# Kernel tuning notes

Hardware: AMD Instinct MI355X
Metric: run time of the kernel (lower is better)

Reference implementation:

```python
import jax, jax.numpy as jnp
import numpy as np

N_NODES = 100000
N_EDGES = 3200000
N_GRAPHS = 64
DIMS = [512, 1024, 512, 256, 128, 64, 32]
N_CLASSES = 10


def setup_inputs() -> dict:
    key = jax.random.key(0)
    ks = jax.random.split(key, 20)
    inp = {}
    inp['h'] = jax.random.normal(ks[0], (N_NODES, DIMS[0]), dtype=jnp.float32)
    inp['src'] = jax.random.randint(ks[1], (N_EDGES,), 0, N_NODES, dtype=jnp.int32)
    inp['dst'] = jax.random.randint(ks[2], (N_EDGES,), 0, N_NODES, dtype=jnp.int32)
    inp['graph_ids'] = jnp.sort(jax.random.randint(ks[3], (N_NODES,), 0, N_GRAPHS, dtype=jnp.int32))
    # GraphConv weights (glorot-like) and biases for the 6 layers
    for i in range(6):
        fi, fo = DIMS[i], DIMS[i + 1]
        scale = jnp.sqrt(2.0 / (fi + fo)).astype(jnp.float32)
        inp[f'W{i+1}'] = jax.random.normal(ks[4 + i], (fi, fo), dtype=jnp.float32) * scale
        inp[f'b{i+1}'] = jnp.zeros((fo,), dtype=jnp.float32)
    inp['Wc'] = jax.random.normal(ks[12], (DIMS[-1], N_CLASSES), dtype=jnp.float32) * 0.1
    inp['bc'] = jnp.zeros((N_CLASSES,), dtype=jnp.float32)
    return inp


def _graph_conv(h, W, b, src, dst, out_inv_sqrt, in_inv_sqrt):
    """DGL GraphConv, norm='both': D_dst^{-1/2} A (D_src^{-1/2} h) W + b.
    Apply W first when it shrinks the feature dim (DGL's mult-first trick)."""
    fi, fo = W.shape
    if fi > fo:
        h = h @ W  # shrink before aggregating
    h = h * out_inv_sqrt[:, None]
    agg = jax.ops.segment_sum(h[src], dst, num_segments=N_NODES)  # SpMM
    agg = agg * in_inv_sqrt[:, None]
    if fi <= fo:
        agg = agg @ W
    return agg + b


def reference(h, src, dst, graph_ids, W1, b1, W2, b2, W3, b3, W4, b4, W5, b5, W6, b6, Wc, bc):
    ones_e = jnp.ones((N_EDGES,), dtype=jnp.float32)
    out_deg = jax.ops.segment_sum(ones_e, src, num_segments=N_NODES)
    in_deg = jax.ops.segment_sum(ones_e, dst, num_segments=N_NODES)
    out_inv_sqrt = jax.lax.rsqrt(jnp.clip(out_deg, 1.0))  # allow_zero_in_degree -> clamp
    in_inv_sqrt = jax.lax.rsqrt(jnp.clip(in_deg, 1.0))
    for (W, b) in [(W1, b1), (W2, b2), (W3, b3), (W4, b4), (W5, b5), (W6, b6)]:
        h = jax.nn.relu(_graph_conv(h, W, b, src, dst, out_inv_sqrt, in_inv_sqrt))
    # dgl.mean_nodes over batched graph
    sums = jax.ops.segment_sum(h, graph_ids, num_segments=N_GRAPHS)
    counts = jax.ops.segment_sum(jnp.ones((N_NODES,), jnp.float32), graph_ids, num_segments=N_GRAPHS)
    hg = sums / jnp.clip(counts, 1.0)[:, None]
    return hg @ Wc + bc  # [N_GRAPHS, n_classes]
```

## Files before the change

### kernel.cpp

```cpp
#include <hip/hip_runtime.h>

#define N_NODES 100000
#define N_EDGES 3200000
#define N_GRAPHS 64
#define M_PAD   100096
#define CAP     128

typedef unsigned short u16;
typedef __bf16 bf16x8 __attribute__((ext_vector_type(8)));
typedef float f32x4 __attribute__((ext_vector_type(4)));
typedef unsigned int u32x4 __attribute__((ext_vector_type(4)));
typedef __attribute__((address_space(3))) unsigned int lds_u32;
typedef __attribute__((address_space(1))) unsigned int glb_u32;

__device__ inline u16 f2bf(float f) {
  unsigned u = __float_as_uint(f);
  unsigned r = (u + 0x7fffu + ((u >> 16) & 1u)) >> 16;
  return (u16)r;
}
__device__ inline float bf2f(u16 h) {
  return __uint_as_float(((unsigned)h) << 16);
}

__global__ void k_build(const int* __restrict__ src, const int* __restrict__ dst,
                        int* __restrict__ odeg, int* __restrict__ cur,
                        int* __restrict__ colp) {
  int e = blockIdx.x * blockDim.x + threadIdx.x;
  if (e < N_EDGES) {
    int s = src[e], d = dst[e];
    atomicAdd(&odeg[s], 1);
    int pos = atomicAdd(&cur[d], 1);
    if (pos < CAP) colp[(size_t)d * CAP + pos] = s;
  }
}

__global__ void k_rsqrt(const int* __restrict__ odeg, const int* __restrict__ ideg,
                        float* __restrict__ a, float* __restrict__ bI) {
  int v = blockIdx.x * blockDim.x + threadIdx.x;
  if (v < N_NODES) {
    a[v]  = rsqrtf(fmaxf((float)odeg[v], 1.0f));
    bI[v] = rsqrtf(fmaxf((float)ideg[v], 1.0f));
  }
}

__global__ void k_prep(const float* __restrict__ x, const float* __restrict__ ascl,
                       u16* __restrict__ y) {
  int i = blockIdx.x * blockDim.x + threadIdx.x;
  if (i >= N_NODES * 128) return;
  int row = i >> 7;
  float s = ascl[row];
  float4 v = ((const float4*)x)[i];
  uint2 o;
  o.x = (unsigned)f2bf(v.x * s) | ((unsigned)f2bf(v.y * s) << 16);
  o.y = (unsigned)f2bf(v.z * s) | ((unsigned)f2bf(v.w * s) << 16);
  ((uint2*)y)[i] = o;
}

__global__ void k_wt(const float* __restrict__ W, u16* __restrict__ Wt, int fi, int fo) {
  int idx = blockIdx.x * blockDim.x + threadIdx.x;
  if (idx >= fi * fo) return;
  int n = idx / fi, k = idx % fi;
  Wt[idx] = f2bf(W[(size_t)k * fo + n]);
}

template<int BM, int BN, int WM, int WN>
__global__ __launch_bounds__(256) void k_mfma(
    const u16* __restrict__ A, const u16* __restrict__ Wt,
    const float* __restrict__ bias, const float* __restrict__ rowscale,
    u16* __restrict__ C, int N, int K, int flags)
{
  constexpr int BK = 32;
  constexpr int WX = BN / WN;
  constexpr int WY = BM / WM;
  static_assert(WX * WY == 4, "4 waves");
  constexpr int TM = WM / 16;
  constexpr int TN = WN / 16;
  constexpr int CA = BM / 16;
  constexpr int CB = BN / 16;

  __shared__ __align__(1024) u16 As[BM * BK];
  __shared__ __align__(1024) u16 Bs[BN * BK];

  const int tid  = threadIdx.x;
  const int wave = tid >> 6;
  const int lane = tid & 63;
  const int wx = wave % WX;
  const int wy = wave / WX;
  const int bm = blockIdx.y * BM;
  const int bn = blockIdx.x * BN;

  const int lm = lane & 15;
  const int lc = lane >> 4;

  const int srA = (lane >> 2);
  const int spA = lane & 3;
  f32x4 acc[TM][TN] = {};

  for (int k0 = 0; k0 < K; k0 += BK) {
    #pragma unroll
    for (int q0 = 0; q0 < CA; q0 += 4) {
      int q = q0 + wave;
      if (q < CA) {
        int rl = q * 16 + srA;
        int c  = (spA - (rl >> 1)) & 3;
        const u16* g = A + (size_t)(bm + rl) * K + k0 + c * 8;
        __builtin_amdgcn_global_load_lds((const glb_u32*)g, (lds_u32*)(As + q * 512), 16, 0, 0);
      }
    }
    #pragma unroll
    for (int q0 = 0; q0 < CB; q0 += 4) {
      int q = q0 + wave;
      if (q < CB) {
        int rl = q * 16 + srA;
        int c  = (spA - (rl >> 1)) & 3;
        const u16* g = Wt + (size_t)(bn + rl) * K + k0 + c * 8;
        __builtin_amdgcn_global_load_lds((const glb_u32*)g, (lds_u32*)(Bs + q * 512), 16, 0, 0);
      }
    }
    __syncthreads();

    bf16x8 af[TM], bfr[TN];
    #pragma unroll
    for (int i = 0; i < TM; ++i) {
      int rl = wy * WM + i * 16 + lm;
      int p = (lc + (rl >> 1)) & 3;
      af[i] = *(const bf16x8*)(As + rl * 32 + p * 8);
    }
    #pragma unroll
    for (int j = 0; j < TN; ++j) {
      int rl = wx * WN + j * 16 + lm;
      int p = (lc + (rl >> 1)) & 3;
      bfr[j] = *(const bf16x8*)(Bs + rl * 32 + p * 8);
    }
    #pragma unroll
    for (int i = 0; i < TM; ++i)
      #pragma unroll
      for (int j = 0; j < TN; ++j)
        acc[i][j] = __builtin_amdgcn_mfma_f32_16x16x32_bf16(af[i], bfr[j], acc[i][j], 0, 0, 0);
    __syncthreads();
  }

  const bool do_br = flags & 1;
  const bool do_rs = flags & 2;
  #pragma unroll
  for (int i = 0; i < TM; ++i) {
    #pragma unroll
    for (int j = 0; j < TN; ++j) {
      int col = bn + wx * WN + j * 16 + lm;
      float bv = do_br ? bias[col] : 0.f;
      #pragma unroll
      for (int r = 0; r < 4; ++r) {
        int row = bm + wy * WM + i * 16 + lc * 4 + r;
        float v = acc[i][j][r];
        if (do_rs) v *= rowscale[row];
        if (do_br) v = fmaxf(v + bv, 0.f);
        C[(size_t)row * N + col] = f2bf(v);
      }
    }
  }
}

template<int DT>
__global__ __launch_bounds__(256) void k_spmm(
    const int* __restrict__ deg, const int* __restrict__ colp,
    const u16* __restrict__ X, const float* __restrict__ dscale,
    const float* __restrict__ bias, u16* __restrict__ Y,
    int Dfull, int c0, int relu_bias)
{
  constexpr int TPR = DT / 8;
  constexpr int NPB = 256 / TPR;
  int node = blockIdx.x * NPB + threadIdx.x / TPR;
  if (node >= N_NODES) return;
  int c = c0 + (threadIdx.x % TPR) * 8;
  const int* cl = colp + (size_t)node * CAP;
  int e = deg[node];
  float acc[8] = {};
  int j = 0;
  for (; j + 3 < e; j += 4) {
    int u0 = cl[j], u1 = cl[j + 1], u2 = cl[j + 2], u3 = cl[j + 3];
    u32x4 v0 = *(const u32x4*)(X + (size_t)u0 * Dfull + c);
    u32x4 v1 = *(const u32x4*)(X + (size_t)u1 * Dfull + c);
    u32x4 v2 = *(const u32x4*)(X + (size_t)u2 * Dfull + c);
    u32x4 v3 = *(const u32x4*)(X + (size_t)u3 * Dfull + c);
    #pragma unroll
    for (int q = 0; q < 4; ++q) {
      acc[2*q]   += __uint_as_float(v0[q] << 16);
      acc[2*q+1] += __uint_as_float(v0[q] & 0xffff0000u);
      acc[2*q]   += __uint_as_float(v1[q] << 16);
      acc[2*q+1] += __uint_as_float(v1[q] & 0xffff0000u);
      acc[2*q]   += __uint_as_float(v2[q] << 16);
      acc[2*q+1] += __uint_as_float(v2[q] & 0xffff0000u);
      acc[2*q]   += __uint_as_float(v3[q] << 16);
      acc[2*q+1] += __uint_as_float(v3[q] & 0xffff0000u);
    }
  }
  for (; j < e; ++j) {
    int u = cl[j];
    u32x4 v = *(const u32x4*)(X + (size_t)u * Dfull + c);
    #pragma unroll
    for (int q = 0; q < 4; ++q) {
      acc[2*q]   += __uint_as_float(v[q] << 16);
      acc[2*q+1] += __uint_as_float(v[q] & 0xffff0000u);
    }
  }
  float dv = dscale[node];
  #pragma unroll
  for (int q = 0; q < 8; ++q) acc[q] *= dv;
  if (relu_bias) {
    #pragma unroll
    for (int q = 0; q < 8; ++q) acc[q] = fmaxf(acc[q] + bias[c + q], 0.f);
  }
  u32x4 o;
  o[0] = (unsigned)f2bf(acc[0]) | ((unsigned)f2bf(acc[1]) << 16);
  o[1] = (unsigned)f2bf(acc[2]) | ((unsigned)f2bf(acc[3]) << 16);
  o[2] = (unsigned)f2bf(acc[4]) | ((unsigned)f2bf(acc[5]) << 16);
  o[3] = (unsigned)f2bf(acc[6]) | ((unsigned)f2bf(acc[7]) << 16);
  *(u32x4*)(Y + (size_t)node * Dfull + c) = o;
}

__global__ __launch_bounds__(256) void k_pool(const u16* __restrict__ h6,
                                              const int* __restrict__ gid,
                                              float* __restrict__ sums,
                                              float* __restrict__ cnts)
{
  __shared__ float acc[N_GRAPHS * 32];
  __shared__ float cnt[N_GRAPHS];
  int t = threadIdx.x;
  for (int k = t; k < N_GRAPHS * 32; k += 256) acc[k] = 0.f;
  if (t < N_GRAPHS) cnt[t] = 0.f;
  __syncthreads();
  int base = blockIdx.x * 256;
  int c = t & 31;
  int nl = t >> 5;
  for (int p = 0; p < 32; ++p) {
    int node = base + p * 8 + nl;
    if (node < N_NODES) {
      int g = gid[node];
      atomicAdd(&acc[g * 32 + c], bf2f(h6[(size_t)node * 32 + c]));
      if (c == 0) atomicAdd(&cnt[g], 1.0f);
    }
  }
  __syncthreads();
  for (int k = t; k < N_GRAPHS * 32; k += 256)
    if (acc[k] != 0.f) atomicAdd(&sums[k], acc[k]);
  if (t < N_GRAPHS && cnt[t] != 0.f) atomicAdd(&cnts[t], cnt[t]);
}

__global__ void k_final(const float* __restrict__ sums, const float* __restrict__ cnts,
                        const float* __restrict__ Wc, const float* __restrict__ bc,
                        float* __restrict__ out)
{
  int t = threadIdx.x;
  if (t >= N_GRAPHS * 10) return;
  int g = t / 10, cls = t % 10;
  float inv = 1.0f / fmaxf(cnts[g], 1.0f);
  float v = bc[cls];
  #pragma unroll
  for (int k = 0; k < 32; ++k)
    v += sums[g * 32 + k] * inv * Wc[k * 10 + cls];
  out[t] = v;
}

extern "C" void kernel_launch(void* const* d_in, const int* in_sizes, int n_in,
                              void* d_out, int out_size, void* d_ws, size_t ws_size,
                              hipStream_t stream)
{
  const float* h   = (const float*)d_in[0];
  const int*   src = (const int*)d_in[1];
  const int*   dst = (const int*)d_in[2];
  const int*   gid = (const int*)d_in[3];
  const float* W[6]; const float* b[6];
  for (int i = 0; i < 6; ++i) { W[i] = (const float*)d_in[4 + 2 * i]; b[i] = (const float*)d_in[5 + 2 * i]; }
  const float* Wc = (const float*)d_in[16];
  const float* bc = (const float*)d_in[17];
  float* out = (float*)d_out;

  const int FI[6] = {512, 1024, 512, 256, 128, 64};
  const int FO[6] = {1024, 512, 256, 128, 64, 32};

  char* p = (char*)d_ws;
  auto take = [&](size_t bytes) -> void* {
    void* r = (void*)p;
    p += (bytes + 255) & ~(size_t)255;
    return r;
  };
  u16* hb   = (u16*)take((size_t)M_PAD * 512 * 2);
  u16* bufA = (u16*)take((size_t)M_PAD * 512 * 2);
  u16* bufB = (u16*)take((size_t)M_PAD * 1024 * 2);
  u16* Wt[6];
  for (int i = 0; i < 6; ++i) Wt[i] = (u16*)take((size_t)FI[i] * FO[i] * 2);
  int*   colp = (int*)take((size_t)N_NODES * CAP * 4);
  int*   odeg = (int*)take((size_t)N_NODES * 4);
  int*   cur  = (int*)take((size_t)N_NODES * 4);
  float* ascl = (float*)take((size_t)M_PAD * 4);
  float* bscl = (float*)take((size_t)N_NODES * 4);
  float* psum = (float*)take((size_t)N_GRAPHS * 32 * 4);
  float* pcnt = (float*)take((size_t)N_GRAPHS * 4);
  if ((size_t)((char*)p - (char*)d_ws) > ws_size) return;

  hipMemsetAsync(odeg, 0, (size_t)N_NODES * 4 * 2 + 256, stream);
  hipMemsetAsync(psum, 0, (size_t)N_GRAPHS * 32 * 4, stream);
  hipMemsetAsync(pcnt, 0, (size_t)N_GRAPHS * 4, stream);

  k_build<<<(N_EDGES + 255) / 256, 256, 0, stream>>>(src, dst, odeg, cur, colp);
  k_rsqrt<<<(N_NODES + 255) / 256, 256, 0, stream>>>(odeg, cur, ascl, bscl);

  k_prep<<<(N_NODES * 128 + 255) / 256, 256, 0, stream>>>(h, ascl, hb);
  for (int i = 0; i < 6; ++i)
    k_wt<<<(FI[i] * FO[i] + 255) / 256, 256, 0, stream>>>(W[i], Wt[i], FI[i], FO[i]);

  const int GY = M_PAD / 128;
  const int G256 = (N_NODES + 7) / 8;
  const int G128 = (N_NODES + 15) / 16;
  const int G64  = (N_NODES + 31) / 32;
  const int G32  = (N_NODES + 63) / 64;

  k_spmm<256><<<G256, 256, 0, stream>>>(cur, colp, hb, bscl, nullptr, bufA, 512, 0, 0);
  k_spmm<256><<<G256, 256, 0, stream>>>(cur, colp, hb, bscl, nullptr, bufA, 512, 256, 0);
  k_mfma<128,128,64,64><<<dim3(8, GY), 256, 0, stream>>>(bufA, Wt[0], b[0], nullptr, bufB, 1024, 512, 1);

  k_mfma<128,128,64,64><<<dim3(4, GY), 256, 0, stream>>>(bufB, Wt[1], nullptr, ascl, bufA, 512, 1024, 2);
  k_spmm<256><<<G256, 256, 0, stream>>>(cur, colp, bufA, bscl, b[1], hb, 512, 0, 1);
  k_spmm<256><<<G256, 256, 0, stream>>>(cur, colp, bufA, bscl, b[1], hb, 512, 256, 1);

  k_mfma<128,128,64,64><<<dim3(2, GY), 256, 0, stream>>>(hb, Wt[2], nullptr, ascl, bufA, 256, 512, 2);
  k_spmm<256><<<G256, 256, 0, stream>>>(cur, colp, bufA, bscl, b[2], hb, 256, 0, 1);

  k_mfma<128,128,64,64><<<dim3(1, GY), 256, 0, stream>>>(hb, Wt[3], nullptr, ascl, bufA, 128, 256, 2);
  k_spmm<128><<<G128, 256, 0, stream>>>(cur, colp, bufA, bscl, b[3], hb, 128, 0, 1);

  k_mfma<128,64,64,32><<<dim3(1, GY), 256, 0, stream>>>(hb, Wt[4], nullptr, ascl, bufA, 64, 128, 2);
  k_spmm<64><<<G64, 256, 0, stream>>>(cur, colp, bufA, bscl, b[4], hb, 64, 0, 1);

  k_mfma<128,32,64,16><<<dim3(1, GY), 256, 0, stream>>>(hb, Wt[5], nullptr, ascl, bufA, 32, 64, 2);
  k_spmm<32><<<G32, 256, 0, stream>>>(cur, colp, bufA, bscl, b[5], hb, 32, 0, 1);

  k_pool<<<(N_NODES + 255) / 256, 256, 0, stream>>>(hb, gid, psum, pcnt);
  k_final<<<1, 640, 0, stream>>>(psum, pcnt, Wc, bc, out);
}
```

Before: 2.550 ms.

## Map one wavefront per node in SpMM and split edges across lanes

The SpMM kernel now gives each node a full 64-lane wavefront. When the feature width is below 512, the spare lanes process different neighbour edges in parallel, and the partial sums are combined with xor shuffles. This is meant to raise memory-level parallelism and cut the serial edge loop for the narrow layers. The two half-width launches for the 512-wide layers merge into one, and the edge count is now clamped to CAP. Output and adjacency stores become nontemporal, at the cost of shuffle-reduction overhead and idle lanes during the final write.

```diff
diff --git a/kernel.cpp b/kernel.cpp
--- a/kernel.cpp
+++ b/kernel.cpp
@@ -30,7 +30,7 @@
     int s = src[e], d = dst[e];
     atomicAdd(&odeg[s], 1);
     int pos = atomicAdd(&cur[d], 1);
-    if (pos < CAP) colp[(size_t)d * CAP + pos] = s;
+    if (pos < CAP) __builtin_nontemporal_store(s, &colp[(size_t)d * CAP + pos]);
   }
 }
 
@@ -160,28 +160,32 @@
   }
 }
 
-template<int DT>
+template<int D>
 __global__ __launch_bounds__(256) void k_spmm(
     const int* __restrict__ deg, const int* __restrict__ colp,
     const u16* __restrict__ X, const float* __restrict__ dscale,
-    const float* __restrict__ bias, u16* __restrict__ Y,
-    int Dfull, int c0, int relu_bias)
-{
-  constexpr int TPR = DT / 8;
-  constexpr int NPB = 256 / TPR;
-  int node = blockIdx.x * NPB + threadIdx.x / TPR;
-  if (node >= N_NODES) return;
-  int c = c0 + (threadIdx.x % TPR) * 8;
+    const float* __restrict__ bias, u16* __restrict__ Y, int relu_bias)
+{
+  constexpr int TPR = D / 8;
+  constexpr int EPW = 64 / TPR;
+  const int lane = threadIdx.x & 63;
+  const int node = blockIdx.x * 4 + (threadIdx.x >> 6);
+  const int g = lane / TPR;
+  const int c = (lane % TPR) * 8;
   const int* cl = colp + (size_t)node * CAP;
   int e = deg[node];
+  e = e < CAP ? e : CAP;
   float acc[8] = {};
   int j = 0;
-  for (; j + 3 < e; j += 4) {
-    int u0 = cl[j], u1 = cl[j + 1], u2 = cl[j + 2], u3 = cl[j + 3];
-    u32x4 v0 = *(const u32x4*)(X + (size_t)u0 * Dfull + c);
-    u32x4 v1 = *(const u32x4*)(X + (size_t)u1 * Dfull + c);
-    u32x4 v2 = *(const u32x4*)(X + (size_t)u2 * Dfull + c);
-    u32x4 v3 = *(const u32x4*)(X + (size_t)u3 * Dfull + c);
+  for (; j + 4 * EPW <= e; j += 4 * EPW) {
+    int u0 = cl[j + g];
+    int u1 = cl[j + g + EPW];
+    int u2 = cl[j + g + 2 * EPW];
+    int u3 = cl[j + g + 3 * EPW];
+    u32x4 v0 = *(const u32x4*)(X + (size_t)u0 * D + c);
+    u32x4 v1 = *(const u32x4*)(X + (size_t)u1 * D + c);
+    u32x4 v2 = *(const u32x4*)(X + (size_t)u2 * D + c);
+    u32x4 v3 = *(const u32x4*)(X + (size_t)u3 * D + c);
     #pragma unroll
     for (int q = 0; q < 4; ++q) {
       acc[2*q]   += __uint_as_float(v0[q] << 16);
@@ -194,28 +198,39 @@
       acc[2*q+1] += __uint_as_float(v3[q] & 0xffff0000u);
     }
   }
-  for (; j < e; ++j) {
-    int u = cl[j];
-    u32x4 v = *(const u32x4*)(X + (size_t)u * Dfull + c);
-    #pragma unroll
-    for (int q = 0; q < 4; ++q) {
-      acc[2*q]   += __uint_as_float(v[q] << 16);
-      acc[2*q+1] += __uint_as_float(v[q] & 0xffff0000u);
-    }
-  }
-  float dv = dscale[node];
-  #pragma unroll
-  for (int q = 0; q < 8; ++q) acc[q] *= dv;
-  if (relu_bias) {
-    #pragma unroll
-    for (int q = 0; q < 8; ++q) acc[q] = fmaxf(acc[q] + bias[c + q], 0.f);
-  }
-  u32x4 o;
-  o[0] = (unsigned)f2bf(acc[0]) | ((unsigned)f2bf(acc[1]) << 16);
-  o[1] = (unsigned)f2bf(acc[2]) | ((unsigned)f2bf(acc[3]) << 16);
-  o[2] = (unsigned)f2bf(acc[4]) | ((unsigned)f2bf(acc[5]) << 16);
-  o[3] = (unsigned)f2bf(acc[6]) | ((unsigned)f2bf(acc[7]) << 16);
-  *(u32x4*)(Y + (size_t)node * Dfull + c) = o;
+  for (; j < e; j += EPW) {
+    if (j + g < e) {
+      int u = cl[j + g];
+      u32x4 v = *(const u32x4*)(X + (size_t)u * D + c);
+      #pragma unroll
+      for (int q = 0; q < 4; ++q) {
+        acc[2*q]   += __uint_as_float(v[q] << 16);
+        acc[2*q+1] += __uint_as_float(v[q] & 0xffff0000u);
+      }
+    }
+  }
+  if constexpr (EPW > 1) {
+    #pragma unroll
+    for (int off = TPR; off < 64; off <<= 1) {
+      #pragma unroll
+      for (int q = 0; q < 8; ++q) acc[q] += __shfl_xor(acc[q], off);
+    }
+  }
+  if (lane < TPR) {
+    float dv = dscale[node];
+    #pragma unroll
+    for (int q = 0; q < 8; ++q) acc[q] *= dv;
+    if (relu_bias) {
+      #pragma unroll
+      for (int q = 0; q < 8; ++q) acc[q] = fmaxf(acc[q] + bias[c + q], 0.f);
+    }
+    u32x4 o;
+    o[0] = (unsigned)f2bf(acc[0]) | ((unsigned)f2bf(acc[1]) << 16);
+    o[1] = (unsigned)f2bf(acc[2]) | ((unsigned)f2bf(acc[3]) << 16);
+    o[2] = (unsigned)f2bf(acc[4]) | ((unsigned)f2bf(acc[5]) << 16);
+    o[3] = (unsigned)f2bf(acc[6]) | ((unsigned)f2bf(acc[7]) << 16);
+    __builtin_nontemporal_store(o, (u32x4*)(Y + (size_t)node * D + c));
+  }
 }
 
 __global__ __launch_bounds__(256) void k_pool(const u16* __restrict__ h6,
@@ -310,30 +325,25 @@
     k_wt<<<(FI[i] * FO[i] + 255) / 256, 256, 0, stream>>>(W[i], Wt[i], FI[i], FO[i]);
 
   const int GY = M_PAD / 128;
-  const int G256 = (N_NODES + 7) / 8;
-  const int G128 = (N_NODES + 15) / 16;
-  const int G64  = (N_NODES + 31) / 32;
-  const int G32  = (N_NODES + 63) / 64;
-
-  k_spmm<256><<<G256, 256, 0, stream>>>(cur, colp, hb, bscl, nullptr, bufA, 512, 0, 0);
-  k_spmm<256><<<G256, 256, 0, stream>>>(cur, colp, hb, bscl, nullptr, bufA, 512, 256, 0);
+  const int GS = N_NODES / 4;
+
+  k_spmm<512><<<GS, 256, 0, stream>>>(cur, colp, hb, bscl, nullptr, bufA, 0);
   k_mfma<128,128,64,64><<<dim3(8, GY), 256, 0, stream>>>(bufA, Wt[0], b[0], nullptr, bufB, 1024, 512, 1);
 
   k_mfma<128,128,64,64><<<dim3(4, GY), 256, 0, stream>>>(bufB, Wt[1], nullptr, ascl, bufA, 512, 1024, 2);
-  k_spmm<256><<<G256, 256, 0, stream>>>(cur, colp, bufA, bscl, b[1], hb, 512, 0, 1);
-  k_spmm<256><<<G256, 256, 0, stream>>>(cur, colp, bufA, bscl, b[1], hb, 512, 256, 1);
+  k_spmm<512><<<GS, 256, 0, stream>>>(cur, colp, bufA, bscl, b[1], hb, 1);
 
   k_mfma<128,128,64,64><<<dim3(2, GY), 256, 0, stream>>>(hb, Wt[2], nullptr, ascl, bufA, 256, 512, 2);
-  k_spmm<256><<<G256, 256, 0, stream>>>(cur, colp, bufA, bscl, b[2], hb, 256, 0, 1);
+  k_spmm<256><<<GS, 256, 0, stream>>>(cur, colp, bufA, bscl, b[2], hb, 1);
 
   k_mfma<128,128,64,64><<<dim3(1, GY), 256, 0, stream>>>(hb, Wt[3], nullptr, ascl, bufA, 128, 256, 2);
-  k_spmm<128><<<G128, 256, 0, stream>>>(cur, colp, bufA, bscl, b[3], hb, 128, 0, 1);
+  k_spmm<128><<<GS, 256, 0, stream>>>(cur, colp, bufA, bscl, b[3], hb, 1);
 
   k_mfma<128,64,64,32><<<dim3(1, GY), 256, 0, stream>>>(hb, Wt[4], nullptr, ascl, bufA, 64, 128, 2);
-  k_spmm<64><<<G64, 256, 0, stream>>>(cur, colp, bufA, bscl, b[4], hb, 64, 0, 1);
+  k_spmm<64><<<GS, 256, 0, stream>>>(cur, colp, bufA, bscl, b[4], hb, 1);
 
   k_mfma<128,32,64,16><<<dim3(1, GY), 256, 0, stream>>>(hb, Wt[5], nullptr, ascl, bufA, 32, 64, 2);
-  k_spmm<32><<<G32, 256, 0, stream>>>(cur, colp, bufA, bscl, b[5], hb, 32, 0, 1);
+  k_spmm<32><<<GS, 256, 0, stream>>>(cur, colp, bufA, bscl, b[5], hb, 1);
 
   k_pool<<<(N_NODES + 255) / 256, 256, 0, stream>>>(hb, gid, psum, pcnt);
   k_final<<<1, 640, 0, stream>>>(psum, pcnt, Wc, bc, out);
```

New measurement: 2.571 ms. No clear change (+0.8%).
